# Kernel tuning notes

Measured on AMD Instinct MI355X. Metric: run time of the kernel, lower is better.

The kernel has to match this reference:

```python
import jax, jax.numpy as jnp
import numpy as np

B, G, A, C = 128, 16, 8732, 21
THR = 0.5        # overlap_threshold
NEG_POS = 3      # neg_pos_ratio
VAR0, VAR1 = 0.1, 0.2  # loc_variance


def center_to_point(b):
    cxcy, wh = b[:, :2], b[:, 2:]
    return jnp.concatenate([cxcy - wh / 2, cxcy + wh / 2], axis=-1)


def iou_matrix(a, b):
    # a: [G,4], b: [A,4] point coords (x1,y1,x2,y2) -> [G,A]
    tl = jnp.maximum(a[:, None, :2], b[None, :, :2])
    br = jnp.minimum(a[:, None, 2:], b[None, :, 2:])
    wh = jnp.clip(br - tl, 0.0)
    inter = wh[..., 0] * wh[..., 1]
    area_a = (a[:, 2] - a[:, 0]) * (a[:, 3] - a[:, 1])
    area_b = (b[:, 2] - b[:, 0]) * (b[:, 3] - b[:, 1])
    return inter / (area_a[:, None] + area_b[None, :] - inter)


def encode(anchors, gt_pt):
    # anchors [A,4] (cx,cy,w,h); gt_pt [A,4] point coords
    g_cxcy = (gt_pt[:, :2] + gt_pt[:, 2:]) / 2
    g_wh = gt_pt[:, 2:] - gt_pt[:, :2]
    d_cxcy = (g_cxcy - anchors[:, :2]) / (anchors[:, 2:] * VAR0)
    d_wh = jnp.log(g_wh / anchors[:, 2:]) / VAR1
    return jnp.concatenate([d_cxcy, d_wh], axis=-1)


def match(boxes, labels, anchors, anchors_pt):
    # boxes [G,4] point coords, labels [G] int
    iou = iou_matrix(boxes, anchors_pt)           # [G,A]
    anchor_index = jnp.argmax(iou, axis=1)        # best anchor per gt, [G]
    gt_overlap = jnp.max(iou, axis=0)             # best gt overlap per anchor, [A]
    gt_index = jnp.argmax(iou, axis=0)            # best gt per anchor, [A]
    gt_overlap = gt_overlap.at[anchor_index].set(1.0)
    for i in range(G):
        gt_index = gt_index.at[anchor_index[i]].set(i)
    gt_coords = boxes[gt_index]                   # [A,4]
    loc = encode(anchors, gt_coords)              # [A,4]
    conf = labels[gt_index] + 1                   # [A], 0 reserved for background
    conf = jnp.where(gt_overlap < THR, 0, conf)
    return loc, conf


def setup_inputs() -> dict:
    key = jax.random.key(0)
    k1, k2, k3, k4, k5, k6, k7 = jax.random.split(key, 7)
    predict_offset_coords = jax.random.normal(k1, (B, A, 4), jnp.float32)
    predict_confidences = jax.random.normal(k2, (B, A, C), jnp.float32)
    # valid gt boxes: centers in [0.2,0.8], sizes in [0.05,0.3]
    c = jax.random.uniform(k3, (B, G, 2)) * 0.6 + 0.2
    s = jax.random.uniform(k4, (B, G, 2)) * 0.25 + 0.05
    target_boxes = jnp.concatenate([c - s / 2, c + s / 2], axis=-1)
    target_labels = jax.random.randint(k5, (B, G), 0, C - 1).astype(jnp.int32)
    # anchors in center-coord form (cx,cy,w,h), strictly positive w,h
    acx = jax.random.uniform(k6, (A, 2)) * 0.9 + 0.05
    awh = jax.random.uniform(k7, (A, 2)) * 0.25 + 0.05
    anchors = jnp.concatenate([acx, awh], axis=-1)
    return {"predict_offset_coords": predict_offset_coords,
            "predict_confidences": predict_confidences,
            "target_boxes": target_boxes,
            "target_labels": target_labels,
            "anchors": anchors}


def reference(predict_offset_coords, predict_confidences, target_boxes, target_labels, anchors):
    anchors_pt = center_to_point(anchors)
    loc_t, conf_t = jax.vmap(match, in_axes=(0, 0, None, None))(
        target_boxes, target_labels, anchors, anchors_pt)
    # labels are built without grad in the original (fresh tensors)
    loc_t = jax.lax.stop_gradient(loc_t)
    conf_t = jax.lax.stop_gradient(conf_t)

    is_pos = conf_t > 0                            # [B,A]
    # smooth L1 (beta=1), summed over positive anchors
    diff = predict_offset_coords - loc_t
    ad = jnp.abs(diff)
    sl1 = jnp.where(ad < 1.0, 0.5 * diff * diff, ad - 0.5)
    loss_loc = jnp.sum(sl1 * is_pos[..., None])

    num_pos = jnp.sum(is_pos, axis=1, keepdims=True)      # [B,1]
    n_total = jnp.sum(num_pos).astype(jnp.float32)
    num_neg = jnp.minimum(NEG_POS * num_pos, A - 1)        # [B,1]

    logp = jax.nn.log_softmax(predict_confidences, axis=-1)
    nll = -jnp.take_along_axis(logp, conf_t[..., None], axis=-1)[..., 0]  # [B,A]

    # hard-negative mining via double argsort
    aux = jnp.where(is_pos, 0.0, nll)
    order = jnp.argsort(-aux, axis=1)
    rank = jnp.argsort(order, axis=1)
    is_neg = rank < num_neg

    sel = jnp.logical_or(is_pos, is_neg)
    loss_cls = jnp.sum(jnp.where(sel, nll, 0.0))
    return loss_loc / n_total, loss_cls / n_total
```

## Files before the change

kernel.cpp:

```cpp
#include <hip/hip_runtime.h>
#include <math.h>

#define B_ 128
#define G_ 16
#define A_ 8732
#define C_ 21
#define THR_ 0.5f
#define NEG_POS_ 3
#define VAR0_ 0.1f
#define VAR1_ 0.2f

#define BA_   (B_ * A_)
#define NTH_  (BA_ / 4)
#define NBLK_ ((NTH_ + 255) / 256)

struct Accum { float loss_loc; float loss_cls; int n_total; int pad; };

__global__ void k_init(Accum* acc) {
    acc->loss_loc = 0.f;
    acc->loss_cls = 0.f;
    acc->n_total  = 0;
}

__global__ __launch_bounds__(512) void k_match(
    const float* __restrict__ tboxes,
    const int*   __restrict__ tlabels,
    const float* __restrict__ anchors,
    int*         __restrict__ match,
    int*         __restrict__ num_pos,
    Accum*                    acc)
{
    const int b    = blockIdx.x;
    const int tid  = threadIdx.x;
    const int lane = tid & 63;
    const int w    = tid >> 6;

    __shared__ float         s_ov[A_];
    __shared__ unsigned char s_gi[A_];
    __shared__ float s_boxlds[G_ * 4];
    __shared__ int   s_lab[G_];
    __shared__ unsigned long long s_gb[8 * G_];
    __shared__ int   s_forced[G_];
    __shared__ int   s_cnt[8];

    if (tid < G_ * 4) s_boxlds[tid] = tboxes[b * G_ * 4 + tid];
    if (tid < G_)     s_lab[tid]    = tlabels[b * G_ + tid];
    __syncthreads();

    float bx0[G_], by0[G_], bx1[G_], by1[G_], bar[G_];
    #pragma unroll
    for (int g = 0; g < G_; ++g) {
        bx0[g] = s_boxlds[g * 4 + 0];
        by0[g] = s_boxlds[g * 4 + 1];
        bx1[g] = s_boxlds[g * 4 + 2];
        by1[g] = s_boxlds[g * 4 + 3];
        bar[g] = (bx1[g] - bx0[g]) * (by1[g] - by0[g]);
    }

    unsigned long long gb[G_];
    #pragma unroll
    for (int g = 0; g < G_; ++g) gb[g] = 0ull;

    for (int a = tid; a < A_; a += 512) {
        float4 an = ((const float4*)anchors)[a];
        float ax0 = an.x - an.z * 0.5f, ay0 = an.y - an.w * 0.5f;
        float ax1 = an.x + an.z * 0.5f, ay1 = an.y + an.w * 0.5f;
        float area_b = (ax1 - ax0) * (ay1 - ay0);
        float bov = -1.f; int bg = 0;
        #pragma unroll
        for (int g = 0; g < G_; ++g) {
            float tlx = fmaxf(bx0[g], ax0);
            float tly = fmaxf(by0[g], ay0);
            float brx = fminf(bx1[g], ax1);
            float bry = fminf(by1[g], ay1);
            float wdt = fmaxf(brx - tlx, 0.f);
            float hgt = fmaxf(bry - tly, 0.f);
            float inter = wdt * hgt;
            float iou = inter / (bar[g] + area_b - inter);
            if (iou > bov) { bov = iou; bg = g; }
            unsigned long long pk =
                ((unsigned long long)__float_as_uint(iou) << 32) |
                (unsigned)(~(unsigned)a);
            if (pk > gb[g]) gb[g] = pk;
        }
        s_ov[a] = bov;
        s_gi[a] = (unsigned char)bg;
    }

    #pragma unroll
    for (int g = 0; g < G_; ++g) {
        #pragma unroll
        for (int off = 32; off > 0; off >>= 1) {
            unsigned long long o = __shfl_down(gb[g], off);
            if (o > gb[g]) gb[g] = o;
        }
    }
    if (lane == 0) {
        #pragma unroll
        for (int g = 0; g < G_; ++g) s_gb[w * G_ + g] = gb[g];
    }
    __syncthreads();
    if (tid < G_) {
        unsigned long long m = 0ull;
        #pragma unroll
        for (int wv = 0; wv < 8; ++wv) {
            unsigned long long v = s_gb[wv * G_ + tid];
            if (v > m) m = v;
        }
        s_forced[tid] = (int)(~(unsigned)(m & 0xFFFFFFFFull));
    }
    __syncthreads();
    if (tid == 0) {
        for (int g = 0; g < G_; ++g) {
            int a = s_forced[g];
            s_ov[a] = 1.0f;
            s_gi[a] = (unsigned char)g;
        }
    }
    __syncthreads();

    int cnt = 0;
    for (int a = tid; a < A_; a += 512) {
        float ov = s_ov[a];
        int g = s_gi[a];
        int conf = (ov < THR_) ? 0 : (s_lab[g] + 1);
        match[b * A_ + a] = conf | (g << 8);
        cnt += (conf > 0);
    }
    #pragma unroll
    for (int off = 32; off > 0; off >>= 1) cnt += __shfl_down(cnt, off);
    if (lane == 0) s_cnt[w] = cnt;
    __syncthreads();
    if (tid == 0) {
        int t = 0;
        #pragma unroll
        for (int wv = 0; wv < 8; ++wv) t += s_cnt[wv];
        num_pos[b] = t;
        atomicAdd(&acc->n_total, t);
    }
}

__global__ __launch_bounds__(256) void k_loss(
    const float* __restrict__ pred_off,
    const float* __restrict__ pred_conf,
    const float* __restrict__ tboxes,
    const float* __restrict__ anchors,
    const int*   __restrict__ match,
    float*       __restrict__ aux,
    float*       __restrict__ part_loc,
    float*       __restrict__ part_cls)
{
    const int tid  = threadIdx.x;
    const int t    = blockIdx.x * 256 + tid;
    const int lane = tid & 63;
    const int w    = tid >> 6;

    __shared__ float s_lloc[4];
    __shared__ float s_pnll[4];

    float lloc = 0.f, pnll = 0.f;

    if (t < NTH_) {
        const float4* cp = (const float4*)pred_conf + (size_t)t * 21;
        float xx[84];
        #pragma unroll
        for (int k = 0; k < 21; ++k) {
            float4 v = cp[k];
            xx[4 * k + 0] = v.x; xx[4 * k + 1] = v.y;
            xx[4 * k + 2] = v.z; xx[4 * k + 3] = v.w;
        }
        int4 mk = ((const int4*)match)[t];
        int mkv[4]; mkv[0] = mk.x; mkv[1] = mk.y; mkv[2] = mk.z; mkv[3] = mk.w;
        float auxv[4];

        #pragma unroll
        for (int j = 0; j < 4; ++j) {
            const int base = 21 * j;
            float m = xx[base];
            #pragma unroll
            for (int c = 1; c < C_; ++c) m = fmaxf(m, xx[base + c]);
            float s = 0.f;
            #pragma unroll
            for (int c = 0; c < C_; ++c) s += __expf(xx[base + c] - m);
            float lse = m + __logf(s);

            int conf = mkv[j] & 0xff;
            int g    = mkv[j] >> 8;
            float xc = xx[base];
            #pragma unroll
            for (int c = 1; c < C_; ++c) xc = (conf == c) ? xx[base + c] : xc;
            float nll = lse - xc;
            bool pos = conf > 0;
            auxv[j] = pos ? 0.f : nll;

            if (pos) {
                pnll += nll;
                int i = t * 4 + j;
                int b = i / A_;
                int a = i - b * A_;
                float4 an = ((const float4*)anchors)[a];
                float4 bx = ((const float4*)tboxes)[b * G_ + g];
                float gcx = (bx.x + bx.z) * 0.5f, gcy = (bx.y + bx.w) * 0.5f;
                float gw = bx.z - bx.x, gh = bx.w - bx.y;
                float l0 = (gcx - an.x) / (an.z * VAR0_);
                float l1 = (gcy - an.y) / (an.w * VAR0_);
                float l2 = logf(gw / an.z) / VAR1_;
                float l3 = logf(gh / an.w) / VAR1_;
                float4 p = ((const float4*)pred_off)[i];
                float d, ad;
                d = p.x - l0; ad = fabsf(d); lloc += (ad < 1.f) ? 0.5f * d * d : ad - 0.5f;
                d = p.y - l1; ad = fabsf(d); lloc += (ad < 1.f) ? 0.5f * d * d : ad - 0.5f;
                d = p.z - l2; ad = fabsf(d); lloc += (ad < 1.f) ? 0.5f * d * d : ad - 0.5f;
                d = p.w - l3; ad = fabsf(d); lloc += (ad < 1.f) ? 0.5f * d * d : ad - 0.5f;
            }
        }
        ((float4*)aux)[t] = make_float4(auxv[0], auxv[1], auxv[2], auxv[3]);
    }

    #pragma unroll
    for (int off = 32; off > 0; off >>= 1) {
        lloc += __shfl_down(lloc, off);
        pnll += __shfl_down(pnll, off);
    }
    if (lane == 0) { s_lloc[w] = lloc; s_pnll[w] = pnll; }
    __syncthreads();
    if (tid == 0) {
        part_loc[blockIdx.x] = s_lloc[0] + s_lloc[1] + s_lloc[2] + s_lloc[3];
        part_cls[blockIdx.x] = s_pnll[0] + s_pnll[1] + s_pnll[2] + s_pnll[3];
    }
}

#define NPT_ 35
__global__ __launch_bounds__(256) void k_select(
    const float* __restrict__ aux,
    const int*   __restrict__ num_pos,
    Accum*                    acc)
{
    const int b    = blockIdx.x;
    const int tid  = threadIdx.x;
    const int lane = tid & 63;
    const int w    = tid >> 6;

    __shared__ int   s_c[2][4];
    __shared__ int   s_cf[4];
    __shared__ float s_sf[4];

    unsigned u[NPT_];
    #pragma unroll
    for (int j = 0; j < NPT_; ++j) {
        int a = tid + j * 256;
        u[j] = (a < A_) ? __float_as_uint(aux[(size_t)b * A_ + a]) : 0u;
    }

    const int K = min(NEG_POS_ * num_pos[b], A_ - 1);

    unsigned lo = 0u, hi = 0x7f800000u;
    int it = 0;
    while (lo < hi) {
        unsigned mid = (lo + hi) >> 1;
        int c = 0;
        #pragma unroll
        for (int j = 0; j < NPT_; ++j) c += (u[j] > mid);
        #pragma unroll
        for (int off = 32; off > 0; off >>= 1) c += __shfl_down(c, off);
        if (lane == 0) s_c[it & 1][w] = c;
        __syncthreads();
        int total = s_c[it & 1][0] + s_c[it & 1][1] + s_c[it & 1][2] + s_c[it & 1][3];
        if (total >= K) lo = mid + 1; else hi = mid;
        ++it;
    }

    int c = 0; float sm = 0.f;
    #pragma unroll
    for (int j = 0; j < NPT_; ++j) {
        if (u[j] > lo) { c++; sm += __uint_as_float(u[j]); }
    }
    #pragma unroll
    for (int off = 32; off > 0; off >>= 1) {
        c  += __shfl_down(c, off);
        sm += __shfl_down(sm, off);
    }
    if (lane == 0) { s_cf[w] = c; s_sf[w] = sm; }
    __syncthreads();
    if (tid == 0) {
        int   ct = s_cf[0] + s_cf[1] + s_cf[2] + s_cf[3];
        float st = s_sf[0] + s_sf[1] + s_sf[2] + s_sf[3];
        float T = __uint_as_float(lo);
        atomicAdd(&acc->loss_cls, st + (float)(K - ct) * T);
    }
}

__global__ __launch_bounds__(256) void k_final(
    const Accum* __restrict__ acc,
    const float* __restrict__ part_loc,
    const float* __restrict__ part_cls,
    float*       __restrict__ out)
{
    const int tid  = threadIdx.x;
    const int lane = tid & 63;
    const int w    = tid >> 6;
    __shared__ float s_l[4], s_cl[4];

    float L = 0.f, Cc = 0.f;
    for (int i = tid; i < NBLK_; i += 256) { L += part_loc[i]; Cc += part_cls[i]; }
    #pragma unroll
    for (int off = 32; off > 0; off >>= 1) {
        L  += __shfl_down(L, off);
        Cc += __shfl_down(Cc, off);
    }
    if (lane == 0) { s_l[w] = L; s_cl[w] = Cc; }
    __syncthreads();
    if (tid == 0) {
        float n = (float)acc->n_total;
        float lloc = s_l[0] + s_l[1] + s_l[2] + s_l[3];
        float lcls = s_cl[0] + s_cl[1] + s_cl[2] + s_cl[3] + acc->loss_cls;
        out[0] = lloc / n;
        out[1] = lcls / n;
    }
}

extern "C" void kernel_launch(void* const* d_in, const int* in_sizes, int n_in,
                              void* d_out, int out_size, void* d_ws, size_t ws_size,
                              hipStream_t stream) {
    const float* pred_off  = (const float*)d_in[0];
    const float* pred_conf = (const float*)d_in[1];
    const float* tboxes    = (const float*)d_in[2];
    const int*   tlabels   = (const int*)  d_in[3];
    const float* anchors   = (const float*)d_in[4];
    float* out = (float*)d_out;

    char* ws = (char*)d_ws;
    int*   match_ws = (int*)ws;     ws += (size_t)BA_ * sizeof(int);
    float* aux_ws   = (float*)ws;   ws += (size_t)BA_ * sizeof(float);
    float* ploc_ws  = (float*)ws;   ws += (size_t)((NBLK_ + 3) & ~3) * sizeof(float);
    float* pcls_ws  = (float*)ws;   ws += (size_t)((NBLK_ + 3) & ~3) * sizeof(float);
    int*   npos_ws  = (int*)ws;     ws += (size_t)((B_ + 3) & ~3) * sizeof(int);
    Accum* acc      = (Accum*)ws;

    k_init<<<1, 1, 0, stream>>>(acc);
    k_match<<<B_, 512, 0, stream>>>(tboxes, tlabels, anchors, match_ws, npos_ws, acc);
    k_loss<<<NBLK_, 256, 0, stream>>>(pred_off, pred_conf, tboxes, anchors,
                                      match_ws, aux_ws, ploc_ws, pcls_ws);
    k_select<<<B_, 256, 0, stream>>>(aux_ws, npos_ws, acc);
    k_final<<<1, 256, 0, stream>>>(acc, ploc_ws, pcls_ws, out);
}
```

Baseline: 232.5 us.

## Stage confidence logits through shared memory with one anchor per thread

Measured after the change: 227.3 us. -2.3%, faster.

```diff
diff --git a/kernel.cpp b/kernel.cpp
--- a/kernel.cpp
+++ b/kernel.cpp
@@ -10,9 +10,8 @@
 #define VAR0_ 0.1f
 #define VAR1_ 0.2f
 
-#define BA_   (B_ * A_)
-#define NTH_  (BA_ / 4)
-#define NBLK_ ((NTH_ + 255) / 256)
+#define BA_    (B_ * A_)
+#define NBLKL_ (BA_ / 256)
 
 struct Accum { float loss_loc; float loss_cls; int n_total; int pad; };
 
@@ -151,70 +150,61 @@
     float*       __restrict__ part_cls)
 {
     const int tid  = threadIdx.x;
-    const int t    = blockIdx.x * 256 + tid;
+    const int i    = blockIdx.x * 256 + tid;
     const int lane = tid & 63;
     const int w    = tid >> 6;
 
-    __shared__ float s_lloc[4];
-    __shared__ float s_pnll[4];
+    __shared__ float4 s_conf4[(256 * C_) / 4];
+    __shared__ float  s_lloc[4];
+    __shared__ float  s_pnll[4];
+
+    const float4* g4 = (const float4*)pred_conf + (size_t)blockIdx.x * (256 * C_ / 4);
+    #pragma unroll
+    for (int k = 0; k < 6; ++k) {
+        int idx = tid + k * 256;
+        if (idx < 256 * C_ / 4) s_conf4[idx] = g4[idx];
+    }
+    __syncthreads();
+
+    const float* sc = (const float*)s_conf4 + tid * C_;
+
+    int mk   = match[i];
+    int conf = mk & 0xff;
+    int g    = mk >> 8;
+
+    float m = sc[0];
+    #pragma unroll
+    for (int c = 1; c < C_; ++c) m = fmaxf(m, sc[c]);
+    float s = 0.f;
+    #pragma unroll
+    for (int c = 0; c < C_; ++c) s += __expf(sc[c] - m);
+    float lse = m + __logf(s);
+
+    float xc  = sc[conf];
+    float nll = lse - xc;
+    bool  pos = conf > 0;
 
     float lloc = 0.f, pnll = 0.f;
-
-    if (t < NTH_) {
-        const float4* cp = (const float4*)pred_conf + (size_t)t * 21;
-        float xx[84];
-        #pragma unroll
-        for (int k = 0; k < 21; ++k) {
-            float4 v = cp[k];
-            xx[4 * k + 0] = v.x; xx[4 * k + 1] = v.y;
-            xx[4 * k + 2] = v.z; xx[4 * k + 3] = v.w;
-        }
-        int4 mk = ((const int4*)match)[t];
-        int mkv[4]; mkv[0] = mk.x; mkv[1] = mk.y; mkv[2] = mk.z; mkv[3] = mk.w;
-        float auxv[4];
-
-        #pragma unroll
-        for (int j = 0; j < 4; ++j) {
-            const int base = 21 * j;
-            float m = xx[base];
-            #pragma unroll
-            for (int c = 1; c < C_; ++c) m = fmaxf(m, xx[base + c]);
-            float s = 0.f;
-            #pragma unroll
-            for (int c = 0; c < C_; ++c) s += __expf(xx[base + c] - m);
-            float lse = m + __logf(s);
-
-            int conf = mkv[j] & 0xff;
-            int g    = mkv[j] >> 8;
-            float xc = xx[base];
-            #pragma unroll
-            for (int c = 1; c < C_; ++c) xc = (conf == c) ? xx[base + c] : xc;
-            float nll = lse - xc;
-            bool pos = conf > 0;
-            auxv[j] = pos ? 0.f : nll;
-
-            if (pos) {
-                pnll += nll;
-                int i = t * 4 + j;
-                int b = i / A_;
-                int a = i - b * A_;
-                float4 an = ((const float4*)anchors)[a];
-                float4 bx = ((const float4*)tboxes)[b * G_ + g];
-                float gcx = (bx.x + bx.z) * 0.5f, gcy = (bx.y + bx.w) * 0.5f;
-                float gw = bx.z - bx.x, gh = bx.w - bx.y;
-                float l0 = (gcx - an.x) / (an.z * VAR0_);
-                float l1 = (gcy - an.y) / (an.w * VAR0_);
-                float l2 = logf(gw / an.z) / VAR1_;
-                float l3 = logf(gh / an.w) / VAR1_;
-                float4 p = ((const float4*)pred_off)[i];
-                float d, ad;
-                d = p.x - l0; ad = fabsf(d); lloc += (ad < 1.f) ? 0.5f * d * d : ad - 0.5f;
-                d = p.y - l1; ad = fabsf(d); lloc += (ad < 1.f) ? 0.5f * d * d : ad - 0.5f;
-                d = p.z - l2; ad = fabsf(d); lloc += (ad < 1.f) ? 0.5f * d * d : ad - 0.5f;
-                d = p.w - l3; ad = fabsf(d); lloc += (ad < 1.f) ? 0.5f * d * d : ad - 0.5f;
-            }
-        }
-        ((float4*)aux)[t] = make_float4(auxv[0], auxv[1], auxv[2], auxv[3]);
+    aux[i] = pos ? 0.f : nll;
+
+    if (pos) {
+        pnll = nll;
+        int b = i / A_;
+        int a = i - b * A_;
+        float4 an = ((const float4*)anchors)[a];
+        float4 bx = ((const float4*)tboxes)[b * G_ + g];
+        float gcx = (bx.x + bx.z) * 0.5f, gcy = (bx.y + bx.w) * 0.5f;
+        float gw = bx.z - bx.x, gh = bx.w - bx.y;
+        float l0 = (gcx - an.x) / (an.z * VAR0_);
+        float l1 = (gcy - an.y) / (an.w * VAR0_);
+        float l2 = logf(gw / an.z) / VAR1_;
+        float l3 = logf(gh / an.w) / VAR1_;
+        float4 p = ((const float4*)pred_off)[i];
+        float d, ad;
+        d = p.x - l0; ad = fabsf(d); lloc += (ad < 1.f) ? 0.5f * d * d : ad - 0.5f;
+        d = p.y - l1; ad = fabsf(d); lloc += (ad < 1.f) ? 0.5f * d * d : ad - 0.5f;
+        d = p.z - l2; ad = fabsf(d); lloc += (ad < 1.f) ? 0.5f * d * d : ad - 0.5f;
+        d = p.w - l3; ad = fabsf(d); lloc += (ad < 1.f) ? 0.5f * d * d : ad - 0.5f;
     }
 
     #pragma unroll
@@ -302,7 +292,7 @@
     __shared__ float s_l[4], s_cl[4];
 
     float L = 0.f, Cc = 0.f;
-    for (int i = tid; i < NBLK_; i += 256) { L += part_loc[i]; Cc += part_cls[i]; }
+    for (int i = tid; i < NBLKL_; i += 256) { L += part_loc[i]; Cc += part_cls[i]; }
     #pragma unroll
     for (int off = 32; off > 0; off >>= 1) {
         L  += __shfl_down(L, off);
@@ -332,15 +322,15 @@
     char* ws = (char*)d_ws;
     int*   match_ws = (int*)ws;     ws += (size_t)BA_ * sizeof(int);
     float* aux_ws   = (float*)ws;   ws += (size_t)BA_ * sizeof(float);
-    float* ploc_ws  = (float*)ws;   ws += (size_t)((NBLK_ + 3) & ~3) * sizeof(float);
-    float* pcls_ws  = (float*)ws;   ws += (size_t)((NBLK_ + 3) & ~3) * sizeof(float);
+    float* ploc_ws  = (float*)ws;   ws += (size_t)((NBLKL_ + 3) & ~3) * sizeof(float);
+    float* pcls_ws  = (float*)ws;   ws += (size_t)((NBLKL_ + 3) & ~3) * sizeof(float);
     int*   npos_ws  = (int*)ws;     ws += (size_t)((B_ + 3) & ~3) * sizeof(int);
     Accum* acc      = (Accum*)ws;
 
     k_init<<<1, 1, 0, stream>>>(acc);
     k_match<<<B_, 512, 0, stream>>>(tboxes, tlabels, anchors, match_ws, npos_ws, acc);
-    k_loss<<<NBLK_, 256, 0, stream>>>(pred_off, pred_conf, tboxes, anchors,
-                                      match_ws, aux_ws, ploc_ws, pcls_ws);
+    k_loss<<<NBLKL_, 256, 0, stream>>>(pred_off, pred_conf, tboxes, anchors,
+                                       match_ws, aux_ws, ploc_ws, pcls_ws);
     k_select<<<B_, 256, 0, stream>>>(aux_ws, npos_ws, acc);
     k_final<<<1, 256, 0, stream>>>(acc, ploc_ws, pcls_ws, out);
 }
```
